# Performance work log

Hardware: AMD Instinct MI355X
Metric: run time of the kernel (lower is better)

## Reference

```python
import jax, jax.numpy as jnp
import numpy as np
from jax import lax

EPS = 1e-5
B, CIN, H, W = 4, 512, 64, 64
CI = CIN // 4          # inter_channels = 128
CQK = CI // 8          # PAM query/key channels = 16
NC = 19                # num_classes


def conv2d(x, w, pad):
    return lax.conv_general_dilated(x, w, (1, 1), [(pad, pad), (pad, pad)],
                                    dimension_numbers=('NCHW', 'OIHW', 'NCHW'))


def bn_relu(x, g, b, m, v):
    # eval-mode BatchNorm2d followed by ReLU
    inv = g * lax.rsqrt(v + EPS)
    return jax.nn.relu(x * inv[None, :, None, None] + (b - m * inv)[None, :, None, None])


def setup_inputs() -> dict:
    key = jax.random.key(0)
    ks = iter(jax.random.split(key, 40))
    rn = lambda shape, s=0.02: (jax.random.normal(next(ks), shape, dtype=jnp.float32) * s)
    ones = lambda n: jnp.ones((n,), jnp.float32)
    zeros = lambda n: jnp.zeros((n,), jnp.float32)
    inp = {
        'x': jax.random.normal(next(ks), (B, CIN, H, W), dtype=jnp.float32),
        # conv_p1: 3x3 conv (no bias) + BN
        'wp1': rn((CI, CIN, 3, 3)),
        'bnp1_w': ones(CI), 'bnp1_b': zeros(CI), 'bnp1_m': zeros(CI), 'bnp1_v': ones(CI),
        # PAM 1x1 convs
        'qw': rn((CQK, CI, 1, 1)), 'qb': zeros(CQK),
        'kw': rn((CQK, CI, 1, 1)), 'kb': zeros(CQK),
        'vw': rn((CI, CI, 1, 1)), 'vb': zeros(CI),
        'pam_gamma': jnp.full((1,), 0.5, jnp.float32),
        # conv_p2
        'wp2': rn((CI, CI, 3, 3)),
        'bnp2_w': ones(CI), 'bnp2_b': zeros(CI), 'bnp2_m': zeros(CI), 'bnp2_v': ones(CI),
        # conv_c1
        'wc1': rn((CI, CIN, 3, 3)),
        'bnc1_w': ones(CI), 'bnc1_b': zeros(CI), 'bnc1_m': zeros(CI), 'bnc1_v': ones(CI),
        'cam_gamma': jnp.full((1,), 0.5, jnp.float32),
        # conv_c2
        'wc2': rn((CI, CI, 3, 3)),
        'bnc2_w': ones(CI), 'bnc2_b': zeros(CI), 'bnc2_m': zeros(CI), 'bnc2_v': ones(CI),
        # classifier heads (dropout is eval-mode identity)
        'cls_w': rn((NC, CI, 1, 1)), 'cls_b': zeros(NC),
        'auxp_w': rn((NC, CI, 1, 1)), 'auxp_b': zeros(NC),
        'auxc_w': rn((NC, CI, 1, 1)), 'auxc_b': zeros(NC),
    }
    return inp


def pam(x, qw, qb, kw, kb, vw, vb, gamma):
    b, c, h, w = x.shape
    n = h * w
    q = (conv2d(x, qw, 0) + qb[None, :, None, None]).reshape(b, -1, n)  # [B,CQK,N]
    k = (conv2d(x, kw, 0) + kb[None, :, None, None]).reshape(b, -1, n)  # [B,CQK,N]
    v = (conv2d(x, vw, 0) + vb[None, :, None, None]).reshape(b, c, n)   # [B,C,N]
    attn = jax.nn.softmax(jnp.einsum('bcn,bcm->bnm', q, k), axis=-1)    # [B,N,N]
    out = jnp.einsum('bcm,bnm->bcn', v, attn).reshape(b, c, h, w)
    return gamma * out + x


def cam(x, gamma):
    b, c, h, w = x.shape
    f = x.reshape(b, c, -1)                                             # [B,C,N]
    attn = jax.nn.softmax(jnp.einsum('bin,bjn->bij', f, f), axis=-1)    # [B,C,C]
    out = jnp.einsum('bij,bjn->bin', attn, f).reshape(b, c, h, w)
    return gamma * out + x


def _forward(x, wp1, bnp1_w, bnp1_b, bnp1_m, bnp1_v,
             qw, qb, kw, kb, vw, vb, pam_gamma,
             wp2, bnp2_w, bnp2_b, bnp2_m, bnp2_v,
             wc1, bnc1_w, bnc1_b, bnc1_m, bnc1_v, cam_gamma,
             wc2, bnc2_w, bnc2_b, bnc2_m, bnc2_v,
             cls_w, cls_b, auxp_w, auxp_b, auxc_w, auxc_b):
    feat_p = bn_relu(conv2d(x, wp1, 1), bnp1_w, bnp1_b, bnp1_m, bnp1_v)
    feat_p = pam(feat_p, qw, qb, kw, kb, vw, vb, pam_gamma)
    feat_p = bn_relu(conv2d(feat_p, wp2, 1), bnp2_w, bnp2_b, bnp2_m, bnp2_v)

    feat_c = bn_relu(conv2d(x, wc1, 1), bnc1_w, bnc1_b, bnc1_m, bnc1_v)
    feat_c = cam(feat_c, cam_gamma)
    feat_c = bn_relu(conv2d(feat_c, wc2, 1), bnc2_w, bnc2_b, bnc2_m, bnc2_v)

    feat = feat_p + feat_c
    out = conv2d(feat, cls_w, 0) + cls_b[None, :, None, None]
    out_p = conv2d(feat_p, auxp_w, 0) + auxp_b[None, :, None, None]
    out_c = conv2d(feat_c, auxc_w, 0) + auxc_b[None, :, None, None]
    return out, out_p, out_c


def reference(x, wp1, bnp1_w, bnp1_b, bnp1_m, bnp1_v,
              qw, qb, kw, kb, vw, vb, pam_gamma,
              wp2, bnp2_w, bnp2_b, bnp2_m, bnp2_v,
              wc1, bnc1_w, bnc1_b, bnc1_m, bnc1_v, cam_gamma,
              wc2, bnc2_w, bnc2_b, bnc2_m, bnc2_v,
              cls_w, cls_b, auxp_w, auxp_b, auxc_w, auxc_b):
    return _forward(x, wp1, bnp1_w, bnp1_b, bnp1_m, bnp1_v,
                    qw, qb, kw, kb, vw, vb, pam_gamma,
                    wp2, bnp2_w, bnp2_b, bnp2_m, bnp2_v,
                    wc1, bnc1_w, bnc1_b, bnc1_m, bnc1_v, cam_gamma,
                    wc2, bnc2_w, bnc2_b, bnc2_m, bnc2_v,
                    cls_w, cls_b, auxp_w, auxp_b, auxc_w, auxc_b)
```

## Files before the change

### kernel.cpp

```cpp
#include <hip/hip_runtime.h>
#include <cstdint>
#include <cstddef>


using s16x8 = __attribute__((ext_vector_type(8))) short;
using u16x8 = __attribute__((ext_vector_type(8))) unsigned short;
using u16x4 = __attribute__((ext_vector_type(4))) unsigned short;
using f32x4 = __attribute__((ext_vector_type(4))) float;
using f32x16 = __attribute__((ext_vector_type(16))) float;
using u32x4v = __attribute__((ext_vector_type(4))) unsigned;

__device__ __forceinline__ f32x4 mfma16(u16x8 a, u16x8 b, f32x4 c) {
  return __builtin_amdgcn_mfma_f32_16x16x32_bf16(
      __builtin_bit_cast(s16x8, a), __builtin_bit_cast(s16x8, b), c, 0, 0, 0);
}
__device__ __forceinline__ f32x16 mfma32(u16x8 a, u16x8 b, f32x16 c) {
  return __builtin_amdgcn_mfma_f32_32x32x16_bf16(
      __builtin_bit_cast(s16x8, a), __builtin_bit_cast(s16x8, b), c, 0, 0, 0);
}
__device__ __forceinline__ float bf2f(unsigned short u) {
  return __builtin_bit_cast(float, (unsigned)u << 16);
}
__device__ __forceinline__ unsigned short f2bf(float f) {
  unsigned u = __builtin_bit_cast(unsigned, f);
  u += 0x7fffu + ((u >> 16) & 1u);
  return (unsigned short)(u >> 16);
}
__device__ __forceinline__ unsigned cvt_pk_bf16(float lo, float hi) {
  unsigned r;
  asm("v_cvt_pk_bf16_f32 %0, %1, %2" : "=v"(r) : "v"(lo), "v"(hi));
  return r;
}
__device__ __forceinline__ u16x8 ld8(const unsigned short* p) {
  return *reinterpret_cast<const u16x8*>(p);
}
__device__ __forceinline__ void gload16(const void* g, void* l) {
  __builtin_amdgcn_global_load_lds(
      (const __attribute__((address_space(1))) void*)g,
      (__attribute__((address_space(3))) void*)l, 16, 0, 0);
}

#define OFF_XT    ((size_t)0)
#define OFF_FP1   ((size_t)19464192)
#define OFF_FC1   ((size_t)24330240)
#define ZERO_BYTES ((size_t)29196288)
#define OFF_FP0   ((size_t)29196288)
#define OFF_FC0   ((size_t)33390592)
#define OFF_FP2   ((size_t)37584896)
#define OFF_FC2   ((size_t)41779200)
#define OFF_WT1   ((size_t)45973504)
#define OFF_WT2   ((size_t)48332800)
#define OFF_QKW   ((size_t)48922624)
#define OFF_VWW   ((size_t)48930816)
#define OFF_HWW   ((size_t)48963584)
#define OFF_BNSS  ((size_t)48988160)
#define OFF_ATTN  ((size_t)48992256)
#define OFF_Q     OFF_FP2
#define OFF_K     (OFF_FP2 + 524288)
#define OFF_V     OFF_FC2

__device__ __forceinline__ int swzkey8(int col) {
  return ((col ^ (col >> 3)) & 7) << 3;
}

__global__ __launch_bounds__(256) void k_xpose(const float* __restrict__ x,
                                               unsigned short* __restrict__ xt) {
  __shared__ float tile[128][65];
  const int t = threadIdx.x;
  const int blk = blockIdx.x;
  const int cb = blk & 3;
  const int h = (blk >> 2) & 63;
  const int b = blk >> 8;
  const float* src = x + ((size_t)(b * 512 + cb * 128) * 64 + h) * 64;
  const int w = t & 63, cr = t >> 6;
  for (int i = 0; i < 32; ++i) tile[cr + i * 4][w] = src[(size_t)(cr + i * 4) * 4096 + w];
  __syncthreads();
  const int w2 = t >> 2, cg = t & 3;
  const int cic = cb * 2 + (cg >> 1);
  const int col = w2 + 1;
  const int key8 = swzkey8(col);
  unsigned short* dst =
      xt + (((size_t)(b * 8 + cic) * 66 + h + 1) * 72 + col) * 64 + (cg & 1) * 32;
#pragma unroll
  for (int j = 0; j < 32; j += 4) {
    const int q0 = (cg & 1) * 32 + j;
    const int srow = (cg >> 1) * 64 + (q0 ^ key8);
    u16x4 pk;
    pk[0] = f2bf(tile[srow + 0][w2]);
    pk[1] = f2bf(tile[srow + 1][w2]);
    pk[2] = f2bf(tile[srow + 2][w2]);
    pk[3] = f2bf(tile[srow + 3][w2]);
    *reinterpret_cast<u16x4*>(dst + j) = pk;
  }
}

struct PackArgs {
  const float *wp1, *wc1, *wp2, *wc2, *qw, *kw, *vw, *clsw, *apw, *acw;
  const float *g1p, *b1p, *m1p, *v1p, *g1c, *b1c, *m1c, *v1c;
  const float *g2p, *b2p, *m2p, *v2p, *g2c, *b2c, *m2c, *v2c;
  unsigned short *wt1, *wt2, *qkw, *vww, *hww;
  float* bnss;
};
__global__ __launch_bounds__(256) void k_pack(PackArgs A) {
  const int i = blockIdx.x * 256 + threadIdx.x;
  const int N1 = 2 * 8 * 9 * 8192;
  const int N2 = N1 + 2 * 2 * 9 * 8192;
  const int N3 = N2 + 2 * 16 * 128;
  const int N4 = N3 + 128 * 128;
  const int N5 = N4 + 3 * 32 * 128;
  const int N6 = N5 + 8 * 128;
  if (i < N1) {
    int e = i & 7, ln = (i >> 3) & 63, q = (i >> 9) & 15;
    int rest = i >> 13;
    int tap = rest % 9, cc = rest / 9;
    int cic = cc & 7, brr = cc >> 3;
    const float* s = brr ? A.wc1 : A.wp1;
    int co = (q >> 2) * 32 + (ln & 31);
    int ci = (q & 3) * 16 + (ln >> 5) * 8 + e;
    A.wt1[i] = f2bf(s[(size_t)(co * 512 + cic * 64 + ci) * 9 + tap]);
  } else if (i < N2) {
    int k = i - N1;
    int e = k & 7, ln = (k >> 3) & 63, q = (k >> 9) & 15;
    int rest = k >> 13;
    int tap = rest % 9, cc = rest / 9;
    int cic = cc & 1, brr = cc >> 1;
    const float* s = brr ? A.wc2 : A.wp2;
    int co = (q >> 2) * 32 + (ln & 31);
    int ci = (q & 3) * 16 + (ln >> 5) * 8 + e;
    A.wt2[k] = f2bf(s[(size_t)(co * 128 + cic * 64 + ci) * 9 + tap]);
  } else if (i < N3) {
    int k = i - N2;
    int ci = k & 127, q = k >> 7;
    const float* s = (q < 16) ? A.qw : A.kw;
    A.qkw[k] = f2bf(s[(q & 15) * 128 + ci]);
  } else if (i < N4) {
    int k = i - N3;
    A.vww[k] = f2bf(A.vw[k]);
  } else if (i < N5) {
    int k = i - N4;
    int ci = k & 127, co = (k >> 7) & 31, hd = k >> 12;
    const float* s = hd == 0 ? A.clsw : (hd == 1 ? A.apw : A.acw);
    A.hww[k] = (co < 19) ? f2bf(s[co * 128 + ci]) : (unsigned short)0;
  } else if (i < N6) {
    int k = i - N5;
    int j = k & 127, seg = k >> 7;
    const float *g, *bb, *mm, *vv;
    switch (seg >> 1) {
      case 0: g = A.g1p; bb = A.b1p; mm = A.m1p; vv = A.v1p; break;
      case 1: g = A.g1c; bb = A.b1c; mm = A.m1c; vv = A.v1c; break;
      case 2: g = A.g2p; bb = A.b2p; mm = A.m2p; vv = A.v2p; break;
      default: g = A.g2c; bb = A.b2c; mm = A.m2c; vv = A.v2c; break;
    }
    float sc = g[j] * rsqrtf(vv[j] + 1e-5f);
    A.bnss[k] = (seg & 1) ? (bb[j] - mm[j] * sc) : sc;
  }
}

template <int NCHUNK>
__global__ __launch_bounds__(512, 2) void k_conv3x3(
    const unsigned short* __restrict__ in0, const unsigned short* __restrict__ in1,
    const unsigned short* __restrict__ wt, const float* __restrict__ bnb,
    unsigned short* __restrict__ out0, unsigned short* __restrict__ out1) {
  __shared__ unsigned short Awin[4 * 72 * 64];
  const int bid = blockIdx.x;
  const int ht = bid & 31;
  const int b = (bid >> 5) & 3;
  const int br = bid >> 7;
  const unsigned short* inp = br ? in1 : in0;
  const unsigned short* wbr = wt + (size_t)br * NCHUNK * 9 * 8192;
  const float* scale = bnb + br * 256;
  const float* shiftp = scale + 128;
  unsigned short* outp = br ? out1 : out0;
  const int tid = threadIdx.x;
  const int lane = tid & 63, wv = tid >> 6;
  const int l31 = lane & 31, hi = lane >> 5;
  const int hi16 = hi * 16;
  const int wn = (wv >> 2) * 64;
  const int cob = (wv & 3) * 32;
  const int rowb = wv >> 2;
  const int h0 = ht * 2;
  const int total = 9 * NCHUNK;
  const size_t wq = (size_t)((wv & 3) * 4) * 512 + lane * 8;

  f32x16 acc[2];
  acc[0] = (f32x16)0.f;
  acc[1] = (f32x16)0.f;
  u16x8 bv0[4], bv1[4];

  auto stageA = [&](int c) {
    const char* sr =
        (const char*)(inp + (((size_t)(b * NCHUNK + c) * 66 + h0) * 72) * 64);
    char* db = (char*)Awin;
#pragma unroll
    for (int i = 0; i < 4; ++i)
      gload16(sr + i * 8192 + tid * 16, db + i * 8192 + tid * 16);
    if (tid < 256) gload16(sr + 32768 + tid * 16, db + 32768 + tid * 16);
  };
  auto loadW = [&](u16x8 (&s)[4], int T) {
    const unsigned short* wtap = wbr + (size_t)T * 8192;
#pragma unroll
    for (int s4 = 0; s4 < 4; ++s4) s[s4] = ld8(wtap + (size_t)s4 * 512 + wq);
  };
  auto compute_tap = [&](int ty, int tx, u16x8 (&bvc)[4], int Tr, bool rld) {
    const char* ab = (const char*)Awin;
    const unsigned short* wr = wbr + (size_t)Tr * 8192;
    int abase[2], akey[2];
#pragma unroll
    for (int mf = 0; mf < 2; ++mf) {
      int col = mf * 32 + l31 + tx;
      abase[mf] = ((rowb + ty) * 72 + col) << 7;
      akey[mf] = ((col ^ (col >> 3)) & 7) << 4;
    }
#pragma unroll
    for (int s = 0; s < 4; ++s) {
      const int ko = s * 32 + hi16;
      u16x8 av0 = *(const u16x8*)(ab + abase[0] + (ko ^ akey[0]));
      u16x8 av1 = *(const u16x8*)(ab + abase[1] + (ko ^ akey[1]));
      u16x8 bb = bvc[s];
      acc[0] = mfma32(av0, bb, acc[0]);
      acc[1] = mfma32(av1, bb, acc[1]);
      if (rld) bvc[s] = ld8(wr + (size_t)s * 512 + wq);
    }
  };
  auto do_chunk = [&](int c, bool odd) {
#pragma unroll
    for (int t = 0; t < 9; ++t) {
      const int T = c * 9 + t;
      const bool rld = (T + 2 < total);
      if (((t & 1) != 0) == odd)
        compute_tap(t / 3, t - (t / 3) * 3, bv0, T + 2, rld);
      else
        compute_tap(t / 3, t - (t / 3) * 3, bv1, T + 2, rld);
    }
  };
  auto boundary = [&](int cn) {
    if (cn < NCHUNK) {
      asm volatile("s_waitcnt lgkmcnt(0)" ::: "memory");
      __builtin_amdgcn_s_barrier();
      stageA(cn);
      asm volatile("s_waitcnt vmcnt(0)" ::: "memory");
      __builtin_amdgcn_s_barrier();
    }
  };

  stageA(0);
  loadW(bv0, 0);
  loadW(bv1, 1);
  asm volatile("s_waitcnt vmcnt(0)" ::: "memory");
  __builtin_amdgcn_s_barrier();

#pragma unroll 1
  for (int c = 0; c < NCHUNK; c += 2) {
    do_chunk(c, false);
    boundary(c + 1);
    do_chunk(c + 1, true);
    boundary(c + 2);
  }

  const int co = cob + l31;
  const float sc = scale[co], sh = shiftp[co];
#pragma unroll
  for (int mf = 0; mf < 2; ++mf)
#pragma unroll
    for (int r = 0; r < 16; ++r) {
      int n = wn + mf * 32 + (r & 3) + 8 * (r >> 2) + 4 * hi;
      float y = acc[mf][r] * sc + sh;
      y = y > 0.f ? y : 0.f;
      outp[((size_t)b * 4096 + (size_t)(h0 + (n >> 6)) * 64 + (n & 63)) * 128 + co] =
          f2bf(y);
    }
}

__global__ __launch_bounds__(256) void k_qkv(
    const unsigned short* __restrict__ fp0, const unsigned short* __restrict__ qkw,
    const unsigned short* __restrict__ vww, const float* __restrict__ qb,
    const float* __restrict__ kb, const float* __restrict__ vb,
    unsigned short* __restrict__ Q, unsigned short* __restrict__ K,
    unsigned short* __restrict__ V2) {
  const int bid = blockIdx.x;
  const int nt = bid & 63, b = bid >> 6;
  const int lane = threadIdx.x & 63, wv = threadIdx.x >> 6;
  const int lg = lane >> 4, l15 = lane & 15;
  const int n = nt * 64 + wv * 16 + l15;
  const unsigned short* fbase = fp0 + ((size_t)b * 4096 + n) * 128 + lg * 8;
  f32x4 vacc[8];
#pragma unroll
  for (int mf = 0; mf < 8; ++mf) vacc[mf] = (f32x4){0.f, 0.f, 0.f, 0.f};
  f32x4 qacc = {0.f, 0.f, 0.f, 0.f}, kacc = {0.f, 0.f, 0.f, 0.f};
#pragma unroll
  for (int kc = 0; kc < 128; kc += 32) {
    u16x8 fb = ld8(fbase + kc);
    u16x8 qa = ld8(qkw + (size_t)l15 * 128 + lg * 8 + kc);
    u16x8 ka = ld8(qkw + 2048 + (size_t)l15 * 128 + lg * 8 + kc);
    qacc = mfma16(qa, fb, qacc);
    kacc = mfma16(ka, fb, kacc);
#pragma unroll
    for (int mf = 0; mf < 8; ++mf) {
      u16x8 va = ld8(vww + (size_t)(mf * 16 + l15) * 128 + lg * 8 + kc);
      vacc[mf] = mfma16(va, fb, vacc[mf]);
    }
  }
  const float LOG2E = 1.44269504088896f;
#pragma unroll
  for (int r = 0; r < 4; ++r) {
    int cq = lg * 4 + r;
    Q[(size_t)(b * 4096 + n) * 16 + cq] = f2bf((qacc[r] + qb[cq]) * LOG2E);
    K[(size_t)(b * 4096 + n) * 16 + cq] = f2bf(kacc[r] + kb[cq]);
  }
#pragma unroll
  for (int mf = 0; mf < 8; ++mf)
#pragma unroll
    for (int r = 0; r < 4; ++r) {
      int c = mf * 16 + lg * 4 + r;
      V2[((size_t)(b * 512 + (n >> 3)) * 128 + c) * 8 + (n & 7)] =
          f2bf(vacc[mf][r] + vb[c]);
    }
}

__global__ __launch_bounds__(512, 1) void k_pam(
    const unsigned short* __restrict__ Q, const unsigned short* __restrict__ K,
    const unsigned short* __restrict__ V2, const unsigned short* __restrict__ fp0,
    unsigned short* __restrict__ fp1, const float* __restrict__ pg) {
  __shared__ float obuf[2][3][16][64][4];
  __shared__ float lred[8][64];
  const int bid = blockIdx.x;
  const int qt = bid & 63, b = bid >> 6;
  const int tid = threadIdx.x;
  const int lane = tid & 63, wv = tid >> 6;
  const int qsub = wv >> 2, mq = wv & 3;
  const int l31 = lane & 31, hi = lane >> 5;
  const int q0 = qt * 64 + qsub * 32;
  const unsigned short* Qp = Q + (size_t)b * 65536;
  const unsigned short* Kp = K + (size_t)b * 65536;
  const unsigned short* Vp = V2 + (size_t)b * 524288;
  const int hi8 = hi * 8;

  const u16x8 qB = ld8(Qp + (size_t)(q0 + l31) * 16 + hi8);

  f32x16 oacc[4];
#pragma unroll
  for (int ch = 0; ch < 4; ++ch) oacc[ch] = (f32x16)0.f;
  float dsum = 0.f;

  auto loadK = [&](int t) -> u16x8 {
    return ld8(Kp + (size_t)(t * 32 + l31) * 16 + hi8);
  };
  auto loadV = [&](int t, u16x8 (&vf)[8]) {
#pragma unroll
    for (int kc = 0; kc < 2; ++kc)
#pragma unroll
      for (int ch = 0; ch < 4; ++ch)
        vf[kc * 4 + ch] =
            ld8(Vp + (size_t)(t * 4 + kc * 2 + hi) * 1024 + (ch * 32 + l31) * 8);
  };
  auto body = [&](u16x8 kA, u16x8 (&vf)[8]) {
    f32x16 pacc = mfma32(kA, qB, (f32x16)0.f);
    float p[16];
#pragma unroll
    for (int r = 0; r < 16; ++r) p[r] = exp2f(pacc[r]);
    dsum += (((p[0] + p[1]) + (p[2] + p[3])) + ((p[4] + p[5]) + (p[6] + p[7]))) +
            (((p[8] + p[9]) + (p[10] + p[11])) + ((p[12] + p[13]) + (p[14] + p[15])));
    unsigned X[8], S[8];
#pragma unroll
    for (int j = 0; j < 8; ++j) X[j] = cvt_pk_bf16(p[2 * j], p[2 * j + 1]);
#pragma unroll
    for (int j = 0; j < 8; ++j) S[j] = __shfl_xor(X[j], 32, 64);
    const bool hc = hi != 0;
    u32x4v w0, w1;
    w0[0] = hc ? S[2] : X[0];
    w0[1] = hc ? S[3] : X[1];
    w0[2] = hc ? X[2] : S[0];
    w0[3] = hc ? X[3] : S[1];
    w1[0] = hc ? S[6] : X[4];
    w1[1] = hc ? S[7] : X[5];
    w1[2] = hc ? X[6] : S[4];
    w1[3] = hc ? X[7] : S[5];
    u16x8 f0 = __builtin_bit_cast(u16x8, w0);
    u16x8 f1 = __builtin_bit_cast(u16x8, w1);
#pragma unroll
    for (int ch = 0; ch < 4; ++ch) oacc[ch] = mfma32(f0, vf[ch], oacc[ch]);
#pragma unroll
    for (int ch = 0; ch < 4; ++ch) oacc[ch] = mfma32(f1, vf[4 + ch], oacc[ch]);
  };

  const int t0 = mq * 32;
  u16x8 kA0 = loadK(t0), kA1;
  u16x8 vf0[8], vf1[8];
  loadV(t0, vf0);
#pragma unroll 1
  for (int t = 0; t < 32; t += 2) {
    kA1 = loadK(t0 + t + 1);
    loadV(t0 + t + 1, vf1);
    body(kA0, vf0);
    if (t + 2 < 32) {
      kA0 = loadK(t0 + t + 2);
      loadV(t0 + t + 2, vf0);
    }
    body(kA1, vf1);
  }

  dsum += __shfl_xor(dsum, 32, 64);
  lred[wv][lane] = dsum;
  if (mq) {
#pragma unroll
    for (int ch = 0; ch < 4; ++ch)
#pragma unroll
      for (int j = 0; j < 4; ++j) {
        f32x4 v = {oacc[ch][4 * j + 0], oacc[ch][4 * j + 1], oacc[ch][4 * j + 2],
                   oacc[ch][4 * j + 3]};
        *reinterpret_cast<f32x4*>(&obuf[qsub][mq - 1][ch * 4 + j][lane][0]) = v;
      }
  }
  __syncthreads();
  if (mq == 0) {
    const float dtot = lred[qsub * 4 + 0][lane] + lred[qsub * 4 + 1][lane] +
                       lred[qsub * 4 + 2][lane] + lred[qsub * 4 + 3][lane];
#pragma unroll
    for (int ch = 0; ch < 4; ++ch)
#pragma unroll
      for (int j = 0; j < 4; ++j) {
        f32x4 s0 = *reinterpret_cast<const f32x4*>(&obuf[qsub][0][ch * 4 + j][lane][0]);
        f32x4 s1 = *reinterpret_cast<const f32x4*>(&obuf[qsub][1][ch * 4 + j][lane][0]);
        f32x4 s2 = *reinterpret_cast<const f32x4*>(&obuf[qsub][2][ch * 4 + j][lane][0]);
#pragma unroll
        for (int r = 0; r < 4; ++r)
          oacc[ch][4 * j + r] += (s0[r] + s1[r]) + s2[r];
      }
    const float rden = 1.f / dtot;
    const float gm = pg[0];
    float rdr[16];
#pragma unroll
    for (int r = 0; r < 16; ++r)
      rdr[r] = __shfl(rden, (r & 3) + 8 * (r >> 2) + 4 * hi, 64);
#pragma unroll
    for (int ch = 0; ch < 4; ++ch) {
      const int c = ch * 32 + l31;
#pragma unroll
      for (int r = 0; r < 16; ++r) {
        const int n = q0 + (r & 3) + 8 * (r >> 2) + 4 * hi;
        const int wp = (n & 63) + 1;
        float o = gm * oacc[ch][r] * rdr[r] +
                  bf2f(fp0[((size_t)b * 4096 + n) * 128 + c]);
        fp1[(((size_t)(b * 2 + (c >> 6)) * 66 + (n >> 6) + 1) * 72 + wp) * 64 +
            ((c & 63) ^ swzkey8(wp))] = f2bf(o);
      }
    }
  }
}

__global__ __launch_bounds__(256) void k_gram(const unsigned short* __restrict__ fc0,
                                              float* __restrict__ Gp) {
  __shared__ float fl[32][132];
  const int bid = blockIdx.x;
  const int nc = bid & 63, b = bid >> 6;
  const int t = threadIdx.x;
  const int i = t >> 1, jh = (t & 1) * 64;
  float acc[64];
#pragma unroll
  for (int j = 0; j < 64; ++j) acc[j] = 0.f;
  for (int c2 = 0; c2 < 2; ++c2) {
    const int n0 = nc * 64 + c2 * 32;
    {
      int nn = t >> 3, kh = t & 7;
      const unsigned short* src = fc0 + ((size_t)b * 4096 + n0 + nn) * 128 + kh * 16;
      u16x8 v0 = ld8(src), v1 = ld8(src + 8);
#pragma unroll
      for (int e = 0; e < 8; ++e) {
        fl[nn][kh * 16 + e] = bf2f(v0[e]);
        fl[nn][kh * 16 + 8 + e] = bf2f(v1[e]);
      }
    }
    __syncthreads();
    for (int nn = 0; nn < 32; ++nn) {
      float fi = fl[nn][i];
      const float4* row = reinterpret_cast<const float4*>(&fl[nn][jh]);
#pragma unroll
      for (int j4 = 0; j4 < 16; ++j4) {
        float4 fv = row[j4];
        acc[4 * j4 + 0] += fi * fv.x;
        acc[4 * j4 + 1] += fi * fv.y;
        acc[4 * j4 + 2] += fi * fv.z;
        acc[4 * j4 + 3] += fi * fv.w;
      }
    }
    __syncthreads();
  }
  float* dst = Gp + (((size_t)b * 64 + nc) * 128 + i) * 128 + jh;
  float4* dst4 = reinterpret_cast<float4*>(dst);
#pragma unroll
  for (int j4 = 0; j4 < 16; ++j4)
    dst4[j4] = make_float4(acc[4 * j4], acc[4 * j4 + 1], acc[4 * j4 + 2], acc[4 * j4 + 3]);
}

__global__ __launch_bounds__(128) void k_softm(const float* __restrict__ Gp,
                                               unsigned short* __restrict__ attn) {
  const int bid = blockIdx.x;
  const int i = bid & 127, b = bid >> 7;
  const int j = threadIdx.x;
  float g = 0.f;
  for (int nc = 0; nc < 64; ++nc) g += Gp[(((size_t)b * 64 + nc) * 128 + i) * 128 + j];
  __shared__ float red[2], red2[2];
  float m = g;
  m = fmaxf(m, __shfl_xor(m, 1, 64));
  m = fmaxf(m, __shfl_xor(m, 2, 64));
  m = fmaxf(m, __shfl_xor(m, 4, 64));
  m = fmaxf(m, __shfl_xor(m, 8, 64));
  m = fmaxf(m, __shfl_xor(m, 16, 64));
  m = fmaxf(m, __shfl_xor(m, 32, 64));
  const int wvi = j >> 6;
  if ((j & 63) == 0) red[wvi] = m;
  __syncthreads();
  m = fmaxf(red[0], red[1]);
  float e = __expf(g - m);
  float s = e;
  s += __shfl_xor(s, 1, 64);
  s += __shfl_xor(s, 2, 64);
  s += __shfl_xor(s, 4, 64);
  s += __shfl_xor(s, 8, 64);
  s += __shfl_xor(s, 16, 64);
  s += __shfl_xor(s, 32, 64);
  if ((j & 63) == 0) red2[wvi] = s;
  __syncthreads();
  s = red2[0] + red2[1];
  attn[((size_t)b * 128 + i) * 128 + j] = f2bf(e / s);
}

__global__ __launch_bounds__(256) void k_camout(
    const unsigned short* __restrict__ fc0, const unsigned short* __restrict__ attn,
    const float* __restrict__ cg, unsigned short* __restrict__ fc1) {
  const int bid = blockIdx.x;
  const int nt = bid & 63, b = bid >> 6;
  const int lane = threadIdx.x & 63, wv = threadIdx.x >> 6;
  const int lg = lane >> 4, l15 = lane & 15;
  const int n = nt * 64 + wv * 16 + l15;
  const unsigned short* fbase = fc0 + ((size_t)b * 4096 + n) * 128 + lg * 8;
  const unsigned short* abase = attn + (size_t)b * 16384 + lg * 8;
  f32x4 acc[8];
#pragma unroll
  for (int mf = 0; mf < 8; ++mf) acc[mf] = (f32x4){0.f, 0.f, 0.f, 0.f};
#pragma unroll
  for (int kc = 0; kc < 128; kc += 32) {
    u16x8 fb = ld8(fbase + kc);
#pragma unroll
    for (int mf = 0; mf < 8; ++mf) {
      u16x8 aa = ld8(abase + (size_t)(mf * 16 + l15) * 128 + kc);
      acc[mf] = mfma16(aa, fb, acc[mf]);
    }
  }
  const float gm = cg[0];
  const int nn = nt * 64 + wv * 16 + l15;
  const int wp = (nn & 63) + 1;
  const int key8 = swzkey8(wp);
#pragma unroll
  for (int mf = 0; mf < 8; ++mf)
#pragma unroll
    for (int r = 0; r < 4; ++r) {
      int c = mf * 16 + lg * 4 + r;
      float o = gm * acc[mf][r] + bf2f(fc0[((size_t)b * 4096 + nn) * 128 + c]);
      fc1[(((size_t)(b * 2 + (c >> 6)) * 66 + (nn >> 6) + 1) * 72 + wp) * 64 +
          ((c & 63) ^ key8)] = f2bf(o);
    }
}

__global__ __launch_bounds__(256) void k_heads(
    const unsigned short* __restrict__ fp2, const unsigned short* __restrict__ fc2,
    const unsigned short* __restrict__ hw, const float* __restrict__ clsb,
    const float* __restrict__ apb, const float* __restrict__ acb,
    float* __restrict__ out) {
  const int bid = blockIdx.x;
  const int nt = bid & 63, b = bid >> 6;
  const int lane = threadIdx.x & 63, wv = threadIdx.x >> 6;
  const int lg = lane >> 4, l15 = lane & 15;
  const int n = nt * 64 + wv * 16 + l15;
  const unsigned short* pb = fp2 + (size_t)(b * 4096 + n) * 128 + lg * 8;
  const unsigned short* cb = fc2 + (size_t)(b * 4096 + n) * 128 + lg * 8;
  f32x4 acc[3][2];
#pragma unroll
  for (int hd = 0; hd < 3; ++hd)
#pragma unroll
    for (int mf = 0; mf < 2; ++mf) acc[hd][mf] = (f32x4){0.f, 0.f, 0.f, 0.f};
#pragma unroll
  for (int kc = 0; kc < 128; kc += 32) {
    u16x8 vp = ld8(pb + kc);
    u16x8 vc = ld8(cb + kc);
    u16x8 vs;
#pragma unroll
    for (int e = 0; e < 8; ++e) vs[e] = f2bf(bf2f(vp[e]) + bf2f(vc[e]));
#pragma unroll
    for (int mf = 0; mf < 2; ++mf) {
      u16x8 a0 = ld8(hw + (size_t)(0 * 32 + mf * 16 + l15) * 128 + lg * 8 + kc);
      u16x8 a1 = ld8(hw + (size_t)(1 * 32 + mf * 16 + l15) * 128 + lg * 8 + kc);
      u16x8 a2 = ld8(hw + (size_t)(2 * 32 + mf * 16 + l15) * 128 + lg * 8 + kc);
      acc[0][mf] = mfma16(a0, vs, acc[0][mf]);
      acc[1][mf] = mfma16(a1, vp, acc[1][mf]);
      acc[2][mf] = mfma16(a2, vc, acc[2][mf]);
    }
  }
  const float* bias[3] = {clsb, apb, acb};
  const size_t hoff[3] = {0, 311296, 622592};
#pragma unroll
  for (int hd = 0; hd < 3; ++hd)
#pragma unroll
    for (int mf = 0; mf < 2; ++mf)
#pragma unroll
      for (int r = 0; r < 4; ++r) {
        int co = mf * 16 + lg * 4 + r;
        if (co < 19)
          out[hoff[hd] + ((size_t)b * 19 + co) * 4096 + n] = acc[hd][mf][r] + bias[hd][co];
      }
}

extern "C" void kernel_launch(void* const* d_in, const int* in_sizes, int n_in,
                              void* d_out, int out_size, void* d_ws, size_t ws_size,
                              hipStream_t stream) {
  (void)in_sizes; (void)n_in; (void)out_size; (void)ws_size;
  const float* x = (const float*)d_in[0];
  const float* wp1 = (const float*)d_in[1];
  const float* g1p = (const float*)d_in[2];
  const float* b1p = (const float*)d_in[3];
  const float* m1p = (const float*)d_in[4];
  const float* v1p = (const float*)d_in[5];
  const float* qw = (const float*)d_in[6];
  const float* qb = (const float*)d_in[7];
  const float* kw = (const float*)d_in[8];
  const float* kb = (const float*)d_in[9];
  const float* vw = (const float*)d_in[10];
  const float* vb = (const float*)d_in[11];
  const float* pamg = (const float*)d_in[12];
  const float* wp2 = (const float*)d_in[13];
  const float* g2p = (const float*)d_in[14];
  const float* b2p = (const float*)d_in[15];
  const float* m2p = (const float*)d_in[16];
  const float* v2p = (const float*)d_in[17];
  const float* wc1 = (const float*)d_in[18];
  const float* g1c = (const float*)d_in[19];
  const float* b1c = (const float*)d_in[20];
  const float* m1c = (const float*)d_in[21];
  const float* v1c = (const float*)d_in[22];
  const float* camg = (const float*)d_in[23];
  const float* wc2 = (const float*)d_in[24];
  const float* g2c = (const float*)d_in[25];
  const float* b2c = (const float*)d_in[26];
  const float* m2c = (const float*)d_in[27];
  const float* v2c = (const float*)d_in[28];
  const float* clsw = (const float*)d_in[29];
  const float* clsb = (const float*)d_in[30];
  const float* apw = (const float*)d_in[31];
  const float* apb = (const float*)d_in[32];
  const float* acw = (const float*)d_in[33];
  const float* acb = (const float*)d_in[34];

  char* ws = (char*)d_ws;
  unsigned short* xt = (unsigned short*)(ws + OFF_XT);
  unsigned short* fp1 = (unsigned short*)(ws + OFF_FP1);
  unsigned short* fc1 = (unsigned short*)(ws + OFF_FC1);
  unsigned short* fp0 = (unsigned short*)(ws + OFF_FP0);
  unsigned short* fc0 = (unsigned short*)(ws + OFF_FC0);
  unsigned short* fp2 = (unsigned short*)(ws + OFF_FP2);
  unsigned short* fc2 = (unsigned short*)(ws + OFF_FC2);
  unsigned short* wt1 = (unsigned short*)(ws + OFF_WT1);
  unsigned short* wt2 = (unsigned short*)(ws + OFF_WT2);
  unsigned short* qkw = (unsigned short*)(ws + OFF_QKW);
  unsigned short* vww = (unsigned short*)(ws + OFF_VWW);
  unsigned short* hww = (unsigned short*)(ws + OFF_HWW);
  float* bnss = (float*)(ws + OFF_BNSS);
  unsigned short* Qb = (unsigned short*)(ws + OFF_Q);
  unsigned short* Kb = (unsigned short*)(ws + OFF_K);
  unsigned short* Vb = (unsigned short*)(ws + OFF_V);
  unsigned short* attnb = (unsigned short*)(ws + OFF_ATTN);
  float* Gp = (float*)(ws + OFF_XT);

  hipMemsetAsync(ws, 0, ZERO_BYTES, stream);

  PackArgs pa;
  pa.wp1 = wp1; pa.wc1 = wc1; pa.wp2 = wp2; pa.wc2 = wc2;
  pa.qw = qw; pa.kw = kw; pa.vw = vw; pa.clsw = clsw; pa.apw = apw; pa.acw = acw;
  pa.g1p = g1p; pa.b1p = b1p; pa.m1p = m1p; pa.v1p = v1p;
  pa.g1c = g1c; pa.b1c = b1c; pa.m1c = m1c; pa.v1c = v1c;
  pa.g2p = g2p; pa.b2p = b2p; pa.m2p = m2p; pa.v2p = v2p;
  pa.g2c = g2c; pa.b2c = b2c; pa.m2c = m2c; pa.v2c = v2c;
  pa.wt1 = wt1; pa.wt2 = wt2; pa.qkw = qkw; pa.vww = vww; pa.hww = hww; pa.bnss = bnss;
  k_pack<<<5892, 256, 0, stream>>>(pa);

  k_xpose<<<1024, 256, 0, stream>>>(x, xt);

  k_conv3x3<8><<<256, 512, 0, stream>>>(xt, xt, wt1, bnss, fp0, fc0);

  k_qkv<<<256, 256, 0, stream>>>(fp0, qkw, vww, qb, kb, vb, Qb, Kb, Vb);
  k_gram<<<256, 256, 0, stream>>>(fc0, Gp);
  k_pam<<<256, 512, 0, stream>>>(Qb, Kb, Vb, fp0, fp1, pamg);
  k_softm<<<512, 128, 0, stream>>>(Gp, attnb);
  k_camout<<<256, 256, 0, stream>>>(fc0, attnb, camg, fc1);

  k_conv3x3<2><<<256, 512, 0, stream>>>(fp1, fc1, wt2, bnss + 512, fp2, fc2);

  k_heads<<<256, 256, 0, stream>>>(fp2, fc2, hww, clsb, apb, acb, (float*)d_out);
}
```

Baseline: 196.1 us.

## Split conv K-chunks across two wave groups and zero only padding borders

The 3x3 conv kernel now splits its input-channel chunks between two groups of four waves, each with its own LDS window. Each wave computes a larger 64x64 output tile with four accumulators, so every A fragment is reused across two weight fragments. The group-1 partial sums are reduced through LDS before the BN+ReLU epilogue. Separately, the full ~29MB memset is replaced by a small kernel that zeroes only the halo rows and columns of the padded buffers, which assumes the interiors are always fully overwritten. This costs more registers and LDS per block and adds a cross-group reduction step.

Result: slower. 246.3 us (+25.6%).

```diff
diff --git a/kernel.cpp b/kernel.cpp
--- a/kernel.cpp
+++ b/kernel.cpp
@@ -43,7 +43,6 @@
 #define OFF_XT    ((size_t)0)
 #define OFF_FP1   ((size_t)19464192)
 #define OFF_FC1   ((size_t)24330240)
-#define ZERO_BYTES ((size_t)29196288)
 #define OFF_FP0   ((size_t)29196288)
 #define OFF_FC0   ((size_t)33390592)
 #define OFF_FP2   ((size_t)37584896)
@@ -61,6 +60,36 @@
 
 __device__ __forceinline__ int swzkey8(int col) {
   return ((col ^ (col >> 3)) & 7) << 3;
+}
+
+__global__ __launch_bounds__(256) void k_padzero(char* ws0) {
+  const int img = blockIdx.x;
+  unsigned short* base;
+  if (img < 32)
+    base = (unsigned short*)(ws0 + OFF_XT) + (size_t)img * 304128;
+  else if (img < 40)
+    base = (unsigned short*)(ws0 + OFF_FP1) + (size_t)(img - 32) * 304128;
+  else
+    base = (unsigned short*)(ws0 + OFF_FC1) + (size_t)(img - 40) * 304128;
+  const u16x8 z = {0, 0, 0, 0, 0, 0, 0, 0};
+#pragma unroll 1
+  for (int it = 0; it < 21; ++it) {
+    int idx = it * 256 + threadIdx.x;
+    if (idx >= 5248) break;
+    int cell = idx >> 3, part = idx & 7;
+    int row, col;
+    if (cell < 72) {
+      row = 0; col = cell;
+    } else if (cell < 144) {
+      row = 65; col = cell - 72;
+    } else {
+      int q = cell - 144;
+      row = 1 + (q >> 3);
+      int cc = q & 7;
+      col = cc ? (64 + cc) : 0;
+    }
+    *(u16x8*)(base + (size_t)(row * 72 + col) * 64 + part * 8) = z;
+  }
 }
 
 __global__ __launch_bounds__(256) void k_xpose(const float* __restrict__ x,
@@ -161,7 +190,7 @@
     const unsigned short* __restrict__ in0, const unsigned short* __restrict__ in1,
     const unsigned short* __restrict__ wt, const float* __restrict__ bnb,
     unsigned short* __restrict__ out0, unsigned short* __restrict__ out1) {
-  __shared__ unsigned short Awin[4 * 72 * 64];
+  __shared__ unsigned short Awin[2 * 4 * 72 * 64];
   const int bid = blockIdx.x;
   const int ht = bid & 31;
   const int b = (bid >> 5) & 3;
@@ -175,35 +204,43 @@
   const int lane = tid & 63, wv = tid >> 6;
   const int l31 = lane & 31, hi = lane >> 5;
   const int hi16 = hi * 16;
-  const int wn = (wv >> 2) * 64;
-  const int cob = (wv & 3) * 32;
-  const int rowb = wv >> 2;
+  const int group = wv >> 2, w = wv & 3;
+  const int wn = (w & 1) * 64, cob = (w >> 1) * 64;
+  const int rowb = w & 1;
   const int h0 = ht * 2;
-  const int total = 9 * NCHUNK;
-  const size_t wq = (size_t)((wv & 3) * 4) * 512 + lane * 8;
-
-  f32x16 acc[2];
-  acc[0] = (f32x16)0.f;
-  acc[1] = (f32x16)0.f;
-  u16x8 bv0[4], bv1[4];
-
-  auto stageA = [&](int c) {
-    const char* sr =
-        (const char*)(inp + (((size_t)(b * NCHUNK + c) * 66 + h0) * 72) * 64);
-    char* db = (char*)Awin;
-#pragma unroll
-    for (int i = 0; i < 4; ++i)
-      gload16(sr + i * 8192 + tid * 16, db + i * 8192 + tid * 16);
-    if (tid < 256) gload16(sr + 32768 + tid * 16, db + 32768 + tid * 16);
+  const int CPG = NCHUNK / 2;
+  const int TPG = CPG * 9;
+  const int c0 = group * CPG;
+  const unsigned short* wgrp = wbr + (size_t)c0 * 9 * 8192;
+  const int gtid = tid & 255;
+  const int wq = (w >> 1) * 8;
+
+  f32x16 acc[2][2];
+#pragma unroll
+  for (int mf = 0; mf < 2; ++mf)
+#pragma unroll
+    for (int nf = 0; nf < 2; ++nf) acc[mf][nf] = (f32x16)0.f;
+  u16x8 bv0[8], bv1[8];
+
+  auto stageA = [&](int cRel) {
+    const char* sr = (const char*)(
+        inp + (((size_t)(b * NCHUNK + c0 + cRel) * 66 + h0) * 72) * 64);
+    char* db = (char*)Awin + group * 36864;
+#pragma unroll
+    for (int i = 0; i < 9; ++i)
+      gload16(sr + i * 4096 + gtid * 16, db + i * 4096 + gtid * 16);
   };
-  auto loadW = [&](u16x8 (&s)[4], int T) {
-    const unsigned short* wtap = wbr + (size_t)T * 8192;
-#pragma unroll
-    for (int s4 = 0; s4 < 4; ++s4) s[s4] = ld8(wtap + (size_t)s4 * 512 + wq);
+  auto loadW = [&](u16x8 (&s)[8], int Tl) {
+    const unsigned short* wtap = wgrp + (size_t)Tl * 8192;
+#pragma unroll
+    for (int nf = 0; nf < 2; ++nf)
+#pragma unroll
+      for (int s4 = 0; s4 < 4; ++s4)
+        s[nf * 4 + s4] = ld8(wtap + (size_t)(wq + nf * 4 + s4) * 512 + lane * 8);
   };
-  auto compute_tap = [&](int ty, int tx, u16x8 (&bvc)[4], int Tr, bool rld) {
-    const char* ab = (const char*)Awin;
-    const unsigned short* wr = wbr + (size_t)Tr * 8192;
+  auto compute_tap = [&](int ty, int tx, u16x8 (&bvc)[8], int Trl, bool rld) {
+    const char* ab = (const char*)Awin + group * 36864;
+    const unsigned short* wr = wgrp + (size_t)Trl * 8192;
     int abase[2], akey[2];
 #pragma unroll
     for (int mf = 0; mf < 2; ++mf) {
@@ -216,59 +253,87 @@
       const int ko = s * 32 + hi16;
       u16x8 av0 = *(const u16x8*)(ab + abase[0] + (ko ^ akey[0]));
       u16x8 av1 = *(const u16x8*)(ab + abase[1] + (ko ^ akey[1]));
-      u16x8 bb = bvc[s];
-      acc[0] = mfma32(av0, bb, acc[0]);
-      acc[1] = mfma32(av1, bb, acc[1]);
-      if (rld) bvc[s] = ld8(wr + (size_t)s * 512 + wq);
+      acc[0][0] = mfma32(av0, bvc[s], acc[0][0]);
+      acc[0][1] = mfma32(av0, bvc[4 + s], acc[0][1]);
+      acc[1][0] = mfma32(av1, bvc[s], acc[1][0]);
+      acc[1][1] = mfma32(av1, bvc[4 + s], acc[1][1]);
+      if (rld) {
+        bvc[s] = ld8(wr + (size_t)(wq + s) * 512 + lane * 8);
+        bvc[4 + s] = ld8(wr + (size_t)(wq + 4 + s) * 512 + lane * 8);
+      }
     }
   };
-  auto do_chunk = [&](int c, bool odd) {
+
+  stageA(0);
+  loadW(bv0, 0);
+  if (TPG > 1) loadW(bv1, 1);
+  asm volatile("s_waitcnt vmcnt(0)" ::: "memory");
+  __builtin_amdgcn_s_barrier();
+
+#pragma unroll 1
+  for (int c = 0; c < CPG; ++c) {
 #pragma unroll
     for (int t = 0; t < 9; ++t) {
-      const int T = c * 9 + t;
-      const bool rld = (T + 2 < total);
-      if (((t & 1) != 0) == odd)
-        compute_tap(t / 3, t - (t / 3) * 3, bv0, T + 2, rld);
+      const int Tl = c * 9 + t;
+      const bool rld = (Tl + 2 < TPG);
+      if (((c + t) & 1) == 0)
+        compute_tap(t / 3, t - (t / 3) * 3, bv0, Tl + 2, rld);
       else
-        compute_tap(t / 3, t - (t / 3) * 3, bv1, T + 2, rld);
-    }
-  };
-  auto boundary = [&](int cn) {
-    if (cn < NCHUNK) {
+        compute_tap(t / 3, t - (t / 3) * 3, bv1, Tl + 2, rld);
+    }
+    if (c + 1 < CPG) {
       asm volatile("s_waitcnt lgkmcnt(0)" ::: "memory");
       __builtin_amdgcn_s_barrier();
-      stageA(cn);
+      stageA(c + 1);
       asm volatile("s_waitcnt vmcnt(0)" ::: "memory");
       __builtin_amdgcn_s_barrier();
     }
-  };
-
-  stageA(0);
-  loadW(bv0, 0);
-  loadW(bv1, 1);
-  asm volatile("s_waitcnt vmcnt(0)" ::: "memory");
+  }
+
+  asm volatile("s_waitcnt lgkmcnt(0)" ::: "memory");
   __builtin_amdgcn_s_barrier();
-
-#pragma unroll 1
-  for (int c = 0; c < NCHUNK; c += 2) {
-    do_chunk(c, false);
-    boundary(c + 1);
-    do_chunk(c + 1, true);
-    boundary(c + 2);
-  }
-
-  const int co = cob + l31;
-  const float sc = scale[co], sh = shiftp[co];
-#pragma unroll
-  for (int mf = 0; mf < 2; ++mf)
-#pragma unroll
-    for (int r = 0; r < 16; ++r) {
-      int n = wn + mf * 32 + (r & 3) + 8 * (r >> 2) + 4 * hi;
-      float y = acc[mf][r] * sc + sh;
-      y = y > 0.f ? y : 0.f;
-      outp[((size_t)b * 4096 + (size_t)(h0 + (n >> 6)) * 64 + (n & 63)) * 128 + co] =
-          f2bf(y);
-    }
+  f32x4* cbuf = (f32x4*)Awin;
+  if (group == 1) {
+#pragma unroll
+    for (int mf = 0; mf < 2; ++mf)
+#pragma unroll
+      for (int nf = 0; nf < 2; ++nf)
+#pragma unroll
+        for (int jj = 0; jj < 4; ++jj) {
+          f32x4 v = {acc[mf][nf][4 * jj + 0], acc[mf][nf][4 * jj + 1],
+                     acc[mf][nf][4 * jj + 2], acc[mf][nf][4 * jj + 3]};
+          cbuf[((w * 16 + mf * 8 + nf * 4 + jj) * 64) + lane] = v;
+        }
+  }
+  asm volatile("s_waitcnt lgkmcnt(0)" ::: "memory");
+  __builtin_amdgcn_s_barrier();
+  if (group == 0) {
+#pragma unroll
+    for (int mf = 0; mf < 2; ++mf)
+#pragma unroll
+      for (int nf = 0; nf < 2; ++nf)
+#pragma unroll
+        for (int jj = 0; jj < 4; ++jj) {
+          f32x4 o = cbuf[((w * 16 + mf * 8 + nf * 4 + jj) * 64) + lane];
+#pragma unroll
+          for (int r = 0; r < 4; ++r) acc[mf][nf][4 * jj + r] += o[r];
+        }
+#pragma unroll
+    for (int nf = 0; nf < 2; ++nf) {
+      const int co = cob + nf * 32 + l31;
+      const float sc = scale[co], sh = shiftp[co];
+#pragma unroll
+      for (int mf = 0; mf < 2; ++mf)
+#pragma unroll
+        for (int r = 0; r < 16; ++r) {
+          int n = wn + mf * 32 + (r & 3) + 8 * (r >> 2) + 4 * hi;
+          float y = acc[mf][nf][r] * sc + sh;
+          y = y > 0.f ? y : 0.f;
+          outp[((size_t)b * 4096 + (size_t)(h0 + (n >> 6)) * 64 + (n & 63)) * 128 +
+               co] = f2bf(y);
+        }
+    }
+  }
 }
 
 __global__ __launch_bounds__(256) void k_qkv(
@@ -670,7 +735,7 @@
   unsigned short* attnb = (unsigned short*)(ws + OFF_ATTN);
   float* Gp = (float*)(ws + OFF_XT);
 
-  hipMemsetAsync(ws, 0, ZERO_BYTES, stream);
+  k_padzero<<<48, 256, 0, stream>>>(ws);
 
   PackArgs pa;
   pa.wp1 = wp1; pa.wc1 = wc1; pa.wp2 = wp2; pa.wc2 = wc2;
```
